# Performance work log

Hardware: AMD Instinct MI355X
Metric: run time of the kernel (lower is better)

## Reference

```python
import jax, jax.numpy as jnp
import numpy as np

B, T, H, I = 256, 1024, 512, 1


def _uniform(key, shape, bound):
    return jax.random.uniform(key, shape, jnp.float32, -bound, bound)


def setup_inputs() -> dict:
    key = jax.random.key(0)
    ks = jax.random.split(key, 11)
    s = 1.0 / np.sqrt(H)
    return {
        "input": jax.random.normal(ks[0], (B, T), jnp.float32),
        "W_ih1": _uniform(ks[1], (3 * H, I), s),
        "W_hh1": _uniform(ks[2], (3 * H, H), s),
        "b_ih1": _uniform(ks[3], (3 * H,), s),
        "b_hh1": _uniform(ks[4], (3 * H,), s),
        "W_ih2": _uniform(ks[5], (3 * H, H), s),
        "W_hh2": _uniform(ks[6], (3 * H, H), s),
        "b_ih2": _uniform(ks[7], (3 * H,), s),
        "b_hh2": _uniform(ks[8], (3 * H,), s),
        "W_out": _uniform(ks[9], (1, H), s),
        "b_out": _uniform(ks[10], (1,), s),
        "future": 0,
    }


def _gru_cell(x, h, W_ih, W_hh, b_ih, b_hh):
    # PyTorch nn.GRUCell: gates ordered (r, z, n)
    gi = x @ W_ih.T + b_ih          # [B, 3H]
    gh = h @ W_hh.T + b_hh          # [B, 3H]
    i_r, i_z, i_n = jnp.split(gi, 3, axis=-1)
    h_r, h_z, h_n = jnp.split(gh, 3, axis=-1)
    r = jax.nn.sigmoid(i_r + h_r)
    z = jax.nn.sigmoid(i_z + h_z)
    n = jnp.tanh(i_n + r * h_n)
    return (1.0 - z) * n + z * h


def _run(input, W_ih1, W_hh1, b_ih1, b_hh1, W_ih2, W_hh2, b_ih2, b_hh2, W_out, b_out, future):
    Bb = input.shape[0]
    h0 = jnp.zeros((Bb, H), input.dtype)

    def step(carry, x_t):  # x_t: [B]
        h1, h2 = carry
        h1 = _gru_cell(x_t[:, None], h1, W_ih1, W_hh1, b_ih1, b_hh1)
        h2 = _gru_cell(h1, h2, W_ih2, W_hh2, b_ih2, b_hh2)
        out = h2 @ W_out.T + b_out  # [B, 1]
        return (h1, h2), out[:, 0]

    (h1, h2), ys = jax.lax.scan(step, (h0, h0), input.T)  # ys: [T, B]
    outs = [ys.T]  # [B, T]
    out = ys[-1][:, None]
    for _ in range(future):
        (h1, h2), o = step((h1, h2), out[:, 0])
        out = o[:, None]
        outs.append(out)
    return jnp.concatenate(outs, axis=1) if future > 0 else outs[0]


def reference(input, W_ih1, W_hh1, b_ih1, b_hh1, W_ih2, W_hh2, b_ih2, b_hh2, W_out, b_out, future):
    return _run(input, W_ih1, W_hh1, b_ih1, b_hh1, W_ih2, W_hh2, b_ih2, b_hh2, W_out, b_out, future)
```

## Files before the change

### kernel.cpp

```cpp
#include <hip/hip_runtime.h>

#define NB 256
#define NT 512
#define TT 1024
#define HH 512
#define BATCH 256

using v8s   = __attribute__((ext_vector_type(8))) short;
using f32x4 = __attribute__((ext_vector_type(4))) float;

#define O_RZ2I 0
#define O_RZ2H 32768
#define O_NA   65536
#define O_RZ1  98304
#define O_NB   131072
#define O_WOUT 147456
#define O_ZERO 149504
#define O_SCR  149520
#define O_SCRO 161808
#define LDS_BYTES 162064

#define SLOT_SH 524288

__device__ __forceinline__ float sigf(float v)   { return 1.f / (1.f + __expf(-v)); }
__device__ __forceinline__ float tanhf_(float v) { return 2.f / (1.f + __expf(-2.f * v)) - 1.f; }

__device__ __forceinline__ unsigned short bf16_rne(float f) {
    union { float f; unsigned u; } a; a.f = f;
    unsigned r = (a.u + 0x7fffu + ((a.u >> 16) & 1u)) >> 16;
    return (unsigned short)r;
}
__device__ __forceinline__ float bf16_f(unsigned short h) {
    union { unsigned u; float f; } a; a.u = ((unsigned)h) << 16; return a.f;
}
__device__ __forceinline__ f32x4 MF(v8s a, v8s b, f32x4 c) {
    return __builtin_amdgcn_mfma_f32_16x16x32_bf16(a, b, c, 0, 0, 0);
}

#define GST2(addr, val) \
    asm volatile("global_store_short %0, %1, off sc0 sc1" \
                 :: "v"(addr), "v"(val) : "memory");

#define BSTR 512
__device__ __forceinline__ void gridbar(unsigned* barr, int bg, int ug, int tid,
                                        unsigned ep, bool fence) {
    asm volatile("s_waitcnt vmcnt(0)" ::: "memory");
    __syncthreads();
    if (tid == 0) {
        unsigned* sub = barr + bg * BSTR + (ug >> 3) * 32;
        unsigned* grp = barr + bg * BSTR + 256;
        unsigned* flg = barr + bg * BSTR + 288;
        unsigned old = __hip_atomic_fetch_add(sub, 1u, __ATOMIC_RELAXED, __HIP_MEMORY_SCOPE_AGENT);
        if (old + 1 == ep * 8u) {
            unsigned g = __hip_atomic_fetch_add(grp, 1u, __ATOMIC_RELAXED, __HIP_MEMORY_SCOPE_AGENT);
            if (g + 1 == ep * 8u)
                __hip_atomic_store(flg, ep, __ATOMIC_RELAXED, __HIP_MEMORY_SCOPE_AGENT);
        }
        while (__hip_atomic_load(flg, __ATOMIC_RELAXED, __HIP_MEMORY_SCOPE_AGENT) < ep)
            __builtin_amdgcn_s_sleep(2);
        if (fence)
            __builtin_amdgcn_fence(__ATOMIC_ACQUIRE, "agent");
    }
    __syncthreads();
}

__global__ __launch_bounds__(256) void k_transpose(const float* __restrict__ x,
                                                   float* __restrict__ xT) {
    __shared__ float tile[64][65];
    const int bt = blockIdx.x, bb = blockIdx.y;
    const int lt = threadIdx.x & 63, lb = threadIdx.x >> 6;
    #pragma unroll 4
    for (int i = 0; i < 16; ++i) {
        int row = lb + i * 4;
        tile[row][lt] = x[(size_t)(bb * 64 + row) * TT + bt * 64 + lt];
    }
    __syncthreads();
    #pragma unroll 4
    for (int i = 0; i < 16; ++i) {
        int row = lb + i * 4;
        xT[(size_t)(bt * 64 + row) * BATCH + bb * 64 + lt] = tile[lt][row];
    }
}

__global__ __launch_bounds__(NT, 1) void gru_mfma(
    const float* __restrict__ xT,
    const float* __restrict__ Wih1, const float* __restrict__ Whh1,
    const float* __restrict__ bih1, const float* __restrict__ bhh1,
    const float* __restrict__ Wih2, const float* __restrict__ Whh2,
    const float* __restrict__ bih2, const float* __restrict__ bhh2,
    const float* __restrict__ Wout, const float* __restrict__ bout,
    float* __restrict__ out,
    unsigned short* __restrict__ hws,
    unsigned* __restrict__ barr,
    int rmask, int invmask)
{
    extern __shared__ char lds_b[];
    const int tid = threadIdx.x, blk = blockIdx.x;
    const int bg = blk >> 6, ug = blk & 63;
    const int u0 = ug * 8;

    for (int i = tid; i < 16 * 512; i += NT) {
        int n = i >> 9, k = i & 511;
        int row = (n < 8) ? (u0 + n) : (HH + u0 + (n - 8));
        float f = Wih2[(size_t)row * HH + k];
        unsigned short hi = bf16_rne(f), lo = bf16_rne(f - bf16_f(hi));
        int s = k >> 5, g = (k >> 3) & 3, j = k & 7, ln = g * 16 + n;
        int base = O_RZ2I + s * 2048 + ln * 16 + j * 2;
        *(unsigned short*)(lds_b + base) = hi;
        *(unsigned short*)(lds_b + base + 1024) = lo;
    }
    for (int i = tid; i < 16 * 512; i += NT) {
        int n = i >> 9, k = i & 511;
        int row = (n < 8) ? (u0 + n) : (HH + u0 + (n - 8));
        float f = Whh2[(size_t)row * HH + k];
        unsigned short hi = bf16_rne(f), lo = bf16_rne(f - bf16_f(hi));
        int s = k >> 5, g = (k >> 3) & 3, j = k & 7, ln = g * 16 + n;
        int base = O_RZ2H + s * 2048 + ln * 16 + j * 2;
        *(unsigned short*)(lds_b + base) = hi;
        *(unsigned short*)(lds_b + base + 1024) = lo;
    }
    for (int i = tid; i < 16 * 512; i += NT) {
        int n = i >> 9, k = i & 511;
        float f = (n < 8) ? Wih2[(size_t)(2 * HH + u0 + n) * HH + k]
                          : Whh1[(size_t)(2 * HH + u0 + (n - 8)) * HH + k];
        unsigned short hi = bf16_rne(f), lo = bf16_rne(f - bf16_f(hi));
        int s = k >> 5, g = (k >> 3) & 3, j = k & 7, ln = g * 16 + n;
        int base = O_NA + s * 2048 + ln * 16 + j * 2;
        *(unsigned short*)(lds_b + base) = hi;
        *(unsigned short*)(lds_b + base + 1024) = lo;
    }
    for (int i = tid; i < 16 * 512; i += NT) {
        int n = i >> 9, k = i & 511;
        int row = (n < 8) ? (u0 + n) : (HH + u0 + (n - 8));
        float f = Whh1[(size_t)row * HH + k];
        unsigned short hi = bf16_rne(f), lo = bf16_rne(f - bf16_f(hi));
        int s = k >> 5, g = (k >> 3) & 3, j = k & 7, ln = g * 16 + n;
        int base = O_RZ1 + s * 2048 + ln * 16 + j * 2;
        *(unsigned short*)(lds_b + base) = hi;
        *(unsigned short*)(lds_b + base + 1024) = lo;
    }
    for (int i = tid; i < 8 * 512; i += NT) {
        int c = i >> 9, k = i & 511;
        float f = Whh2[(size_t)(2 * HH + u0 + c) * HH + k];
        unsigned short hi = bf16_rne(f), lo = bf16_rne(f - bf16_f(hi));
        int s = k >> 5, g = (k >> 3) & 3, j = k & 7;
        int base = O_NB + s * 1024 + (g * 8 + c) * 16 + j * 2;
        *(unsigned short*)(lds_b + base) = hi;
        *(unsigned short*)(lds_b + base + 512) = lo;
    }
    for (int k = tid; k < 512; k += NT) {
        float f = Wout[k];
        unsigned short hi = bf16_rne(f), lo = bf16_rne(f - bf16_f(hi));
        int s = k >> 5, g = (k >> 3) & 3, j = k & 7;
        int base = O_WOUT + s * 64 + g * 16 + j * 2;
        *(unsigned short*)(lds_b + base) = hi;
        *(unsigned short*)(lds_b + base + 1024) = lo;
    }
    if (tid < 4) ((unsigned*)(lds_b + O_ZERO))[tid] = 0;

    {
        const int rl = tid >> 3, uo = tid & 7;
        const int b = bg * 64 + rl, u = u0 + uo;
        unsigned short* s0 = hws;
        GST2(s0 + 262144 + (size_t)b * HH + u, 0u);
        GST2(s0 + 393216 + (size_t)b * HH + u, 0u);
        float x0 = xT[b];
        float r = sigf(x0 * Wih1[u] + bih1[u] + bhh1[u]);
        float z = sigf(x0 * Wih1[HH + u] + bih1[HH + u] + bhh1[HH + u]);
        float n = tanhf_(x0 * Wih1[2 * HH + u] + bih1[2 * HH + u] + r * bhh1[2 * HH + u]);
        float h = (1.f - z) * n;
        unsigned short hi = bf16_rne(h), lo = bf16_rne(h - bf16_f(hi));
        GST2(s0 + (size_t)b * HH + u, (unsigned)hi);
        GST2(s0 + 131072 + (size_t)b * HH + u, (unsigned)lo);
    }

    const int w = tid >> 6, lane = tid & 63;
    const int n16 = lane & 15, g4 = lane >> 4;
    const int rt = w & 3, kh = w >> 2;
    const int c = n16, cu = c & 7;
    const int u = u0 + cu;
    const int sbase = kh * 8;

    float b2rz = 0, wx1 = 0, b1rz = 0, bin2_ = 0, bhn2_ = 0, wxn1 = 0, bin1_ = 0, bhn1_ = 0;
    float hprev[4] = {0.f, 0.f, 0.f, 0.f};
    if (kh == 1) {
        b2rz = (c < 8) ? bih2[u] + bhh2[u] : bih2[HH + u] + bhh2[HH + u];
        wx1  = (c < 8) ? Wih1[u] : Wih1[HH + u];
        b1rz = (c < 8) ? bih1[u] + bhh1[u] : bih1[HH + u] + bhh1[HH + u];
        bin2_ = bih2[2 * HH + u]; bhn2_ = bhh2[2 * HH + u];
        wxn1 = Wih1[2 * HH + u]; bin1_ = bih1[2 * HH + u]; bhn1_ = bhh1[2 * HH + u];
        if (c >= 8) {
            #pragma unroll
            for (int j = 0; j < 4; ++j) {
                int b = bg * 64 + rt * 16 + g4 * 4 + j;
                float x0 = xT[b];
                float r = sigf(x0 * Wih1[u] + bih1[u] + bhh1[u]);
                float z = sigf(x0 * Wih1[HH + u] + bih1[HH + u] + bhh1[HH + u]);
                float nn = tanhf_(x0 * Wih1[2 * HH + u] + bih1[2 * HH + u] + r * bhh1[2 * HH + u]);
                hprev[j] = (1.f - z) * nn;
            }
        }
    }
    const float boutv = bout[0];

    const char* Bi = lds_b + O_RZ2I + lane * 16;
    const char* Bh = lds_b + O_RZ2H + lane * 16;
    const char* BA = lds_b + O_NA   + lane * 16;
    const char* B1 = lds_b + O_RZ1  + lane * 16;
    const char* BBh = (n16 < 8) ? lds_b + O_NB + kh * 8192 + (g4 * 8 + n16) * 16
                                : lds_b + O_ZERO;
    const char* BBl = (n16 < 8) ? BBh + 512 : lds_b + O_ZERO;
    const int  bbs  = (n16 < 8) ? 1024 : 0;
    const char* Bo  = (n16 == 0) ? lds_b + O_WOUT + kh * 512 + g4 * 16 : lds_b + O_ZERO;
    const char* Bol = (n16 == 0) ? Bo + 1024 : lds_b + O_ZERO;
    const int  bos  = (n16 == 0) ? 64 : 0;

    float* scr = (float*)(lds_b + O_SCR);
    float* so  = (float*)(lds_b + O_SCRO);

    unsigned ep = 1;
    gridbar(barr, bg, ug, tid, ep, false);

    for (int t = 0; t <= TT; ++t) {
        const unsigned short* __restrict__ slotR = hws + (size_t)(t & rmask) * SLOT_SH;
        unsigned short* __restrict__ slotW = hws + (size_t)((t + 1) & rmask) * SLOT_SH;
        const unsigned short* __restrict__ h1rh = slotR;
        const unsigned short* __restrict__ h1rl = slotR + 131072;
        const unsigned short* __restrict__ h2rh = slotR + 262144;
        const unsigned short* __restrict__ h2rl = slotR + 393216;
        unsigned short* h1wh = slotW;
        unsigned short* h1wl = slotW + 131072;
        unsigned short* h2wh = slotW + 262144;
        unsigned short* h2wl = slotW + 393216;

        const size_t aoff = ((size_t)(bg * 64 + rt * 16 + n16) * HH + (size_t)kh * 256 + g4 * 8);
        const unsigned short* __restrict__ pa1h = h1rh + aoff;
        const unsigned short* __restrict__ pa1l = h1rl + aoff;
        const unsigned short* __restrict__ pa2h = h2rh + aoff;
        const unsigned short* __restrict__ pa2l = h2rl + aoff;

        f32x4 ai = {0.f,0.f,0.f,0.f}, ah = {0.f,0.f,0.f,0.f}, a1v = {0.f,0.f,0.f,0.f};
        f32x4 aA = {0.f,0.f,0.f,0.f}, aB = {0.f,0.f,0.f,0.f}, ao = {0.f,0.f,0.f,0.f};

        #pragma unroll
        for (int sl = 0; sl < 8; ++sl) {
            const int s = sbase + sl;
            const v8s a1h = *(const v8s*)(pa1h + sl * 32);
            const v8s a1l = *(const v8s*)(pa1l + sl * 32);
            const v8s a2h = *(const v8s*)(pa2h + sl * 32);
            const v8s a2l = *(const v8s*)(pa2l + sl * 32);
            v8s bh, bl;
            bh = *(const v8s*)(Bi + s * 2048); bl = *(const v8s*)(Bi + s * 2048 + 1024);
            ai = MF(a1h, bh, ai); ai = MF(a1l, bh, ai); ai = MF(a1h, bl, ai);
            bh = *(const v8s*)(Bh + s * 2048); bl = *(const v8s*)(Bh + s * 2048 + 1024);
            ah = MF(a2h, bh, ah); ah = MF(a2l, bh, ah); ah = MF(a2h, bl, ah);
            bh = *(const v8s*)(BA + s * 2048); bl = *(const v8s*)(BA + s * 2048 + 1024);
            aA = MF(a1h, bh, aA); aA = MF(a1l, bh, aA); aA = MF(a1h, bl, aA);
            bh = *(const v8s*)(B1 + s * 2048); bl = *(const v8s*)(B1 + s * 2048 + 1024);
            a1v = MF(a1h, bh, a1v); a1v = MF(a1l, bh, a1v); a1v = MF(a1h, bl, a1v);
            bh = *(const v8s*)(BBh + sl * bbs); bl = *(const v8s*)(BBl + sl * bbs);
            aB = MF(a2h, bh, aB); aB = MF(a2l, bh, aB); aB = MF(a2h, bl, aB);
            bh = *(const v8s*)(Bo + sl * bos); bl = *(const v8s*)(Bol + sl * bos);
            ao = MF(a2h, bh, ao); ao = MF(a2l, bh, ao); ao = MF(a2h, bl, ao);
        }

        if (kh == 0) {
            #pragma unroll
            for (int j = 0; j < 4; ++j) {
                const int row = g4 * 4 + j;
                scr[(0 * 4 + rt) * 256 + row * 16 + c] = ai[j] + ah[j];
                scr[(1 * 4 + rt) * 256 + row * 16 + c] = a1v[j];
                scr[(2 * 4 + rt) * 256 + row * 16 + c] = aA[j];
            }
            if (c == 0) {
                #pragma unroll
                for (int j = 0; j < 4; ++j) so[rt * 16 + g4 * 4 + j] = ao[j];
            }
        }
        __syncthreads();

        float s2v[4], zz2[4], s1v[4], rr1[4], AAv[4], xvv[4];
        if (kh == 1) {
            #pragma unroll
            for (int j = 0; j < 4; ++j) {
                const int row = g4 * 4 + j;
                const int b = bg * 64 + rt * 16 + row;
                const float AIAH = ai[j] + ah[j] + scr[(0 * 4 + rt) * 256 + row * 16 + c];
                const float A1v  = a1v[j] + scr[(1 * 4 + rt) * 256 + row * 16 + c];
                AAv[j] = aA[j] + scr[(2 * 4 + rt) * 256 + row * 16 + c];
                xvv[j] = (t + 1 < TT) ? xT[(size_t)(t + 1) * BATCH + b] : 0.f;
                s2v[j] = sigf(AIAH + b2rz);
                s1v[j] = sigf(xvv[j] * wx1 + b1rz + A1v);
            }
            #pragma unroll
            for (int j = 0; j < 4; ++j) {
                zz2[j] = __shfl_xor(s2v[j], 8);
                rr1[j] = __shfl_xor(s1v[j], 8);
            }
        }
        __syncthreads();

        if (kh == 0) {
            #pragma unroll
            for (int j = 0; j < 4; ++j) {
                const int row = g4 * 4 + j;
                scr[(0 * 4 + rt) * 256 + row * 16 + c] = aB[j];
            }
        }
        __syncthreads();

        if (kh == 1) {
            #pragma unroll
            for (int j = 0; j < 4; ++j) {
                const int row = g4 * 4 + j;
                const int b = bg * 64 + rt * 16 + row;
                if (c < 8) {
                    if (t < TT) {
                        const float ABv = aB[j] + scr[(0 * 4 + rt) * 256 + row * 16 + c];
                        float n2 = tanhf_(AAv[j] + bin2_ + s2v[j] * (ABv + bhn2_));
                        float hn = (1.f - zz2[j]) * n2 + zz2[j] * hprev[j];
                        hprev[j] = hn;
                        unsigned short hi = bf16_rne(hn), lo = bf16_rne(hn - bf16_f(hi));
                        GST2(h2wh + (size_t)b * HH + u, (unsigned)hi);
                        GST2(h2wl + (size_t)b * HH + u, (unsigned)lo);
                    }
                } else {
                    if (t + 1 < TT) {
                        float n1 = tanhf_(xvv[j] * wxn1 + bin1_ + rr1[j] * (AAv[j] + bhn1_));
                        float hn = (1.f - s1v[j]) * n1 + s1v[j] * hprev[j];
                        hprev[j] = hn;
                        unsigned short hi = bf16_rne(hn), lo = bf16_rne(hn - bf16_f(hi));
                        GST2(h1wh + (size_t)b * HH + u, (unsigned)hi);
                        GST2(h1wl + (size_t)b * HH + u, (unsigned)lo);
                    }
                }
                if (c == 0 && ug == 0 && t >= 1) {
                    float AO = ao[j] + so[rt * 16 + row];
                    out[(size_t)b * TT + (t - 1)] = AO + boutv;
                }
            }
        }
        ++ep;
        gridbar(barr, bg, ug, tid, ep, (t & invmask) == invmask);
    }
}

extern "C" void kernel_launch(void* const* d_in, const int* in_sizes, int n_in,
                              void* d_out, int out_size, void* d_ws, size_t ws_size,
                              hipStream_t stream) {
    const float* x    = (const float*)d_in[0];
    const float* Wih1 = (const float*)d_in[1];
    const float* Whh1 = (const float*)d_in[2];
    const float* bih1 = (const float*)d_in[3];
    const float* bhh1 = (const float*)d_in[4];
    const float* Wih2 = (const float*)d_in[5];
    const float* Whh2 = (const float*)d_in[6];
    const float* bih2 = (const float*)d_in[7];
    const float* bhh2 = (const float*)d_in[8];
    const float* Wout = (const float*)d_in[9];
    const float* bout = (const float*)d_in[10];
    float* outp = (float*)d_out;

    const size_t MB = 1048576;
    size_t avail = (ws_size > MB + 8192) ? ws_size - MB - 8192 : 2 * MB;
    int R = 2;
    while (R < 64 && (size_t)(R * 2) * MB <= avail) R *= 2;
    const int INVP = (R >= 4) ? (R / 2) : 1;

    unsigned short* hws = (unsigned short*)d_ws;
    float* xT      = (float*)((char*)d_ws + (size_t)R * MB);
    unsigned* barr = (unsigned*)((char*)d_ws + (size_t)R * MB + MB);

    hipMemsetAsync((void*)barr, 0, 8192, stream);
    k_transpose<<<dim3(16, 4), 256, 0, stream>>>(x, xT);

    hipFuncSetAttribute((const void*)gru_mfma,
                        hipFuncAttributeMaxDynamicSharedMemorySize, LDS_BYTES);

    int rmask = R - 1, invmask = INVP - 1;
    void* args[] = { (void*)&xT,
                     (void*)&Wih1, (void*)&Whh1, (void*)&bih1, (void*)&bhh1,
                     (void*)&Wih2, (void*)&Whh2, (void*)&bih2, (void*)&bhh2,
                     (void*)&Wout, (void*)&bout,
                     (void*)&outp, (void*)&hws, (void*)&barr,
                     (void*)&rmask, (void*)&invmask };
    hipLaunchCooperativeKernel((void*)gru_mfma, dim3(NB), dim3(NT),
                               args, LDS_BYTES, stream);
}
```

Measured before the change: 11.44 ms.

## Flatten grid barrier, cache RZ weights in registers, merge LDS reduction phases

Replaces the two-level hierarchical grid barrier with a single per-group atomic counter that all 64 blocks spin on. Preloads the r/z gate weight fragments for layers 2 input and hidden into registers once, so the step loop no longer reads them from LDS. Moves the reduction scratch to the start of LDS, which now reuses the weight region after the preload, pads its rows to 20 floats to cut bank conflicts, and writes the aB partial together with the others, removing two __syncthreads per step. The flat counter may see more atomic contention, and the register-held weights raise VGPR pressure.

```diff
diff --git a/kernel.cpp b/kernel.cpp
--- a/kernel.cpp
+++ b/kernel.cpp
@@ -16,8 +16,6 @@
 #define O_NB   131072
 #define O_WOUT 147456
 #define O_ZERO 149504
-#define O_SCR  149520
-#define O_SCRO 161808
 #define LDS_BYTES 162064
 
 #define SLOT_SH 524288
@@ -41,23 +39,15 @@
     asm volatile("global_store_short %0, %1, off sc0 sc1" \
                  :: "v"(addr), "v"(val) : "memory");
 
-#define BSTR 512
-__device__ __forceinline__ void gridbar(unsigned* barr, int bg, int ug, int tid,
+__device__ __forceinline__ void gridbar(unsigned* barr, int bg, int tid,
                                         unsigned ep, bool fence) {
     asm volatile("s_waitcnt vmcnt(0)" ::: "memory");
     __syncthreads();
     if (tid == 0) {
-        unsigned* sub = barr + bg * BSTR + (ug >> 3) * 32;
-        unsigned* grp = barr + bg * BSTR + 256;
-        unsigned* flg = barr + bg * BSTR + 288;
-        unsigned old = __hip_atomic_fetch_add(sub, 1u, __ATOMIC_RELAXED, __HIP_MEMORY_SCOPE_AGENT);
-        if (old + 1 == ep * 8u) {
-            unsigned g = __hip_atomic_fetch_add(grp, 1u, __ATOMIC_RELAXED, __HIP_MEMORY_SCOPE_AGENT);
-            if (g + 1 == ep * 8u)
-                __hip_atomic_store(flg, ep, __ATOMIC_RELAXED, __HIP_MEMORY_SCOPE_AGENT);
-        }
-        while (__hip_atomic_load(flg, __ATOMIC_RELAXED, __HIP_MEMORY_SCOPE_AGENT) < ep)
-            __builtin_amdgcn_s_sleep(2);
+        unsigned* cnt = barr + bg * 64;
+        __hip_atomic_fetch_add(cnt, 1u, __ATOMIC_RELAXED, __HIP_MEMORY_SCOPE_AGENT);
+        while (__hip_atomic_load(cnt, __ATOMIC_RELAXED, __HIP_MEMORY_SCOPE_AGENT) < ep * 64u)
+            __builtin_amdgcn_s_sleep(1);
         if (fence)
             __builtin_amdgcn_fence(__ATOMIC_ACQUIRE, "agent");
     }
@@ -203,8 +193,6 @@
     }
     const float boutv = bout[0];
 
-    const char* Bi = lds_b + O_RZ2I + lane * 16;
-    const char* Bh = lds_b + O_RZ2H + lane * 16;
     const char* BA = lds_b + O_NA   + lane * 16;
     const char* B1 = lds_b + O_RZ1  + lane * 16;
     const char* BBh = (n16 < 8) ? lds_b + O_NB + kh * 8192 + (g4 * 8 + n16) * 16
@@ -215,11 +203,26 @@
     const char* Bol = (n16 == 0) ? Bo + 1024 : lds_b + O_ZERO;
     const int  bos  = (n16 == 0) ? 64 : 0;
 
-    float* scr = (float*)(lds_b + O_SCR);
-    float* so  = (float*)(lds_b + O_SCRO);
+    float* scr = (float*)(lds_b + 0);
+    float* so  = (float*)(lds_b + 32768);
 
     unsigned ep = 1;
-    gridbar(barr, bg, ug, tid, ep, false);
+    gridbar(barr, bg, tid, ep, true);
+
+    v8s RBi[8][2], RBh[8][2];
+    {
+        const char* Bi = lds_b + O_RZ2I + lane * 16;
+        const char* Bh = lds_b + O_RZ2H + lane * 16;
+        #pragma unroll
+        for (int s8 = 0; s8 < 8; ++s8) {
+            const int s = sbase + s8;
+            RBi[s8][0] = *(const v8s*)(Bi + s * 2048);
+            RBi[s8][1] = *(const v8s*)(Bi + s * 2048 + 1024);
+            RBh[s8][0] = *(const v8s*)(Bh + s * 2048);
+            RBh[s8][1] = *(const v8s*)(Bh + s * 2048 + 1024);
+        }
+    }
+    __syncthreads();
 
     for (int t = 0; t <= TT; ++t) {
         const unsigned short* __restrict__ slotR = hws + (size_t)(t & rmask) * SLOT_SH;
@@ -249,11 +252,9 @@
             const v8s a1l = *(const v8s*)(pa1l + sl * 32);
             const v8s a2h = *(const v8s*)(pa2h + sl * 32);
             const v8s a2l = *(const v8s*)(pa2l + sl * 32);
+            ai = MF(a1h, RBi[sl][0], ai); ai = MF(a1l, RBi[sl][0], ai); ai = MF(a1h, RBi[sl][1], ai);
+            ah = MF(a2h, RBh[sl][0], ah); ah = MF(a2l, RBh[sl][0], ah); ah = MF(a2h, RBh[sl][1], ah);
             v8s bh, bl;
-            bh = *(const v8s*)(Bi + s * 2048); bl = *(const v8s*)(Bi + s * 2048 + 1024);
-            ai = MF(a1h, bh, ai); ai = MF(a1l, bh, ai); ai = MF(a1h, bl, ai);
-            bh = *(const v8s*)(Bh + s * 2048); bl = *(const v8s*)(Bh + s * 2048 + 1024);
-            ah = MF(a2h, bh, ah); ah = MF(a2l, bh, ah); ah = MF(a2h, bl, ah);
             bh = *(const v8s*)(BA + s * 2048); bl = *(const v8s*)(BA + s * 2048 + 1024);
             aA = MF(a1h, bh, aA); aA = MF(a1l, bh, aA); aA = MF(a1h, bl, aA);
             bh = *(const v8s*)(B1 + s * 2048); bl = *(const v8s*)(B1 + s * 2048 + 1024);
@@ -268,9 +269,10 @@
             #pragma unroll
             for (int j = 0; j < 4; ++j) {
                 const int row = g4 * 4 + j;
-                scr[(0 * 4 + rt) * 256 + row * 16 + c] = ai[j] + ah[j];
-                scr[(1 * 4 + rt) * 256 + row * 16 + c] = a1v[j];
-                scr[(2 * 4 + rt) * 256 + row * 16 + c] = aA[j];
+                scr[(0 * 4 + rt) * 320 + row * 20 + c] = ai[j] + ah[j];
+                scr[(1 * 4 + rt) * 320 + row * 20 + c] = a1v[j];
+                scr[(2 * 4 + rt) * 320 + row * 20 + c] = aA[j];
+                scr[(3 * 4 + rt) * 320 + row * 20 + c] = aB[j];
             }
             if (c == 0) {
                 #pragma unroll
@@ -279,15 +281,16 @@
         }
         __syncthreads();
 
-        float s2v[4], zz2[4], s1v[4], rr1[4], AAv[4], xvv[4];
         if (kh == 1) {
+            float s2v[4], zz2[4], s1v[4], rr1[4], AAv[4], ABv[4], xvv[4];
             #pragma unroll
             for (int j = 0; j < 4; ++j) {
                 const int row = g4 * 4 + j;
                 const int b = bg * 64 + rt * 16 + row;
-                const float AIAH = ai[j] + ah[j] + scr[(0 * 4 + rt) * 256 + row * 16 + c];
-                const float A1v  = a1v[j] + scr[(1 * 4 + rt) * 256 + row * 16 + c];
-                AAv[j] = aA[j] + scr[(2 * 4 + rt) * 256 + row * 16 + c];
+                const float AIAH = ai[j] + ah[j] + scr[(0 * 4 + rt) * 320 + row * 20 + c];
+                const float A1v  = a1v[j] + scr[(1 * 4 + rt) * 320 + row * 20 + c];
+                AAv[j] = aA[j] + scr[(2 * 4 + rt) * 320 + row * 20 + c];
+                ABv[j] = aB[j] + scr[(3 * 4 + rt) * 320 + row * 20 + c];
                 xvv[j] = (t + 1 < TT) ? xT[(size_t)(t + 1) * BATCH + b] : 0.f;
                 s2v[j] = sigf(AIAH + b2rz);
                 s1v[j] = sigf(xvv[j] * wx1 + b1rz + A1v);
@@ -297,27 +300,13 @@
                 zz2[j] = __shfl_xor(s2v[j], 8);
                 rr1[j] = __shfl_xor(s1v[j], 8);
             }
-        }
-        __syncthreads();
-
-        if (kh == 0) {
-            #pragma unroll
-            for (int j = 0; j < 4; ++j) {
-                const int row = g4 * 4 + j;
-                scr[(0 * 4 + rt) * 256 + row * 16 + c] = aB[j];
-            }
-        }
-        __syncthreads();
-
-        if (kh == 1) {
             #pragma unroll
             for (int j = 0; j < 4; ++j) {
                 const int row = g4 * 4 + j;
                 const int b = bg * 64 + rt * 16 + row;
                 if (c < 8) {
                     if (t < TT) {
-                        const float ABv = aB[j] + scr[(0 * 4 + rt) * 256 + row * 16 + c];
-                        float n2 = tanhf_(AAv[j] + bin2_ + s2v[j] * (ABv + bhn2_));
+                        float n2 = tanhf_(AAv[j] + bin2_ + s2v[j] * (ABv[j] + bhn2_));
                         float hn = (1.f - zz2[j]) * n2 + zz2[j] * hprev[j];
                         hprev[j] = hn;
                         unsigned short hi = bf16_rne(hn), lo = bf16_rne(hn - bf16_f(hi));
@@ -341,7 +330,7 @@
             }
         }
         ++ep;
-        gridbar(barr, bg, ug, tid, ep, (t & invmask) == invmask);
+        gridbar(barr, bg, tid, ep, (t & invmask) == invmask);
     }
 }
 
```

Result: faster. 11.07 ms (-3.2%).
